# Performance work log

Hardware: AMD Instinct MI355X
Metric: run time of the kernel (lower is better)

## Reference

```python
import jax, jax.numpy as jnp
import numpy as np

B, S, HIDDEN, HEAD = 2, 2048, 1024, 16
CHUNK = HIDDEN // HEAD


def setup_inputs() -> dict:
    key = jax.random.key(0)
    ks = jax.random.split(key, 6)
    mk = lambda k, shape, std=1.0: jax.random.normal(k, shape, dtype=jnp.float32) * std
    return {
        "q": mk(ks[0], (B, S, HIDDEN)),
        "k": mk(ks[1], (B, S, HIDDEN)),
        "v": mk(ks[2], (B, S, HIDDEN)),
        "w_q": mk(ks[3], (HIDDEN, HIDDEN), 0.01),
        "w_k": mk(ks[4], (HIDDEN, HIDDEN), 0.01),
        "w_v": mk(ks[5], (HIDDEN, HIDDEN), 0.01),
    }


def _split_heads(x):
    # tf.stack(tf.split(x, head, axis=-1), axis=0): [B,S,HIDDEN] -> [HEAD,B,S,CHUNK]
    b, s, _ = x.shape
    return x.reshape(b, s, HEAD, CHUNK).transpose(2, 0, 1, 3)


def reference(q, k, v, w_q, w_k, w_v):
    emb_q = jnp.matmul(q, w_q)
    emb_k = jnp.matmul(k, w_k)
    emb_v = jnp.matmul(v, w_v)
    mq, mk, mv = _split_heads(emb_q), _split_heads(emb_k), _split_heads(emb_v)  # [H,B,S,C]
    scale = jnp.float32(CHUNK) ** 0.5
    scores = jnp.einsum("hbsc,hbtc->hbst", mq, mk) / scale  # [H,B,S,S]
    attn = jax.nn.softmax(scores, axis=-1)
    # post-softmax causal mask (band_part(-1, 0) == lower triangle) then renormalize
    s = attn.shape[-1]
    tril = jnp.tril(jnp.ones((s, s), dtype=attn.dtype))
    attn = attn * tril
    attn = attn / jnp.sum(attn, axis=3, keepdims=True)
    out = jnp.einsum("hbst,hbtc->hbsc", attn, mv)  # [H,B,S,C]
    # concat heads back on last axis: [H,B,S,C] -> [B,S,HIDDEN]
    return out.transpose(1, 2, 0, 3).reshape(q.shape[0], q.shape[1], HIDDEN)
```

## Files before the change

kernel.cpp:

```cpp
#include <hip/hip_runtime.h>
#include <stdint.h>

#define B_   2
#define S_   2048
#define HID  1024
#define NH   16
#define CH   64
#define MTOT (B_ * S_)
#define NELEM ((size_t)MTOT * HID)
#define WELEM ((size_t)HID * HID)

typedef unsigned short u16;
typedef unsigned int u32;
typedef __attribute__((ext_vector_type(4))) float f32x4;
typedef __attribute__((ext_vector_type(8))) short s16x8;
typedef __attribute__((ext_vector_type(4))) short s16x4;

__device__ __forceinline__ u16 f2bf(float f) {
  union { float f; unsigned u; } v; v.f = f;
  unsigned u = v.u;
  return (u16)((u + 0x7FFFu + ((u >> 16) & 1u)) >> 16);
}

__device__ __forceinline__ f32x4 mfma16(s16x8 a, s16x8 b, f32x4 c) {
  asm("v_mfma_f32_16x16x32_bf16 %0, %1, %2, %0" : "+v"(c) : "v"(a), "v"(b));
  return c;
}

__device__ __forceinline__ f32x4 mfma16z(s16x8 a, s16x8 b, f32x4 c) {
  f32x4 d;
  asm("v_mfma_f32_16x16x32_bf16 %0, %1, %2, %3"
      : "=&v"(d) : "v"(a), "v"(b), "v"(c));
  return d;
}

__device__ __forceinline__ f32x4 mfma16t(s16x8 a, s16x8 b, f32x4 c) {
  asm("v_mfma_f32_16x16x32_bf16 %0, %1, %2, %0" : "+&v"(c) : "v"(a), "v"(b));
  return c;
}

__device__ __forceinline__ f32x4 mfma16k16t(s16x4 a, s16x4 b, f32x4 c) {
  asm("v_mfma_f32_16x16x16_bf16 %0, %1, %2, %0" : "+&v"(c) : "v"(a), "v"(b));
  return c;
}

__device__ __forceinline__ u32 cvtpk(float lo, float hi) {
  u32 r;
  asm("v_cvt_pk_bf16_f32 %0, %1, %2" : "=v"(r) : "v"(lo), "v"(hi));
  return r;
}

__device__ __forceinline__ void mfma_fence() {
  asm volatile("s_nop 7\n\ts_nop 7\n\ts_nop 7" ::: );
}

__device__ __forceinline__ void gload_lds16(const u16* g, u16* l) {
  __builtin_amdgcn_global_load_lds((const __attribute__((address_space(1))) void*)g,
                                   (__attribute__((address_space(3))) void*)l,
                                   16, 0, 0);
}

__global__ __launch_bounds__(256) void k_transposeW(const float* __restrict__ w0,
                                                    const float* __restrict__ w1,
                                                    const float* __restrict__ w2,
                                                    u16* __restrict__ wT) {
  const float* w = (blockIdx.z == 0) ? w0 : (blockIdx.z == 1) ? w1 : w2;
  u16* o = wT + (size_t)blockIdx.z * WELEM;
  __shared__ u16 tile[64][65];
  int x = threadIdx.x & 63, y = threadIdx.x >> 6;
  int r0 = blockIdx.x * 64, c0 = blockIdx.y * 64;
#pragma unroll
  for (int i = 0; i < 16; ++i) {
    int r = i * 4 + y;
    tile[r][x] = f2bf(w[(size_t)(r0 + r) * HID + c0 + x]);
  }
  __syncthreads();
#pragma unroll
  for (int i = 0; i < 16; ++i) {
    int cc = i * 4 + y;
    o[(size_t)(c0 + cc) * HID + r0 + x] = tile[x][cc];
  }
}

__global__ __launch_bounds__(256) void k_gemm(const float* __restrict__ qf32,
                                              const float* __restrict__ kf32,
                                              const float* __restrict__ vf32,
                                              const u16* __restrict__ BTall,
                                              u16* __restrict__ Call,
                                              u16* __restrict__ Vfrag) {
  int lin = blockIdx.x;
  int xcd = lin & 7;
  int chunk = xcd * 96 + (lin >> 3);
  int zz = chunk >> 8;
  int rem = chunk & 255;
  int ty = rem >> 3;
  int tx = rem & 7;

  const float* Af = (zz == 0) ? qf32 : (zz == 1) ? kf32 : vf32;
  const u16* BT = BTall + (size_t)zz * WELEM;
  u16*       C  = Call  + (size_t)zz * NELEM;
  int row0 = ty * 128, col0 = tx * 128;

  __shared__ __align__(16) u16 sA[128 * 32];
  __shared__ __align__(16) u16 sB[128 * 32];

  int t = threadIdx.x;
  int wave = t >> 6, lane = t & 63;
  int lrow = lane & 15, lhi = lane >> 4;
  int wr = wave >> 1, wc = wave & 1;

  f32x4 acc[4][4] = {};

  for (int kt = 0; kt < HID; kt += 32) {
#pragma unroll
    for (int r = 0; r < 2; ++r) {
      int idx = r * 256 + t;
      int srow = idx >> 2, scol = (idx & 3) << 3;
      int ldsoff = (r * 256 + wave * 64) * 8;
      gload_lds16(BT + (size_t)(col0 + srow) * HID + kt + scol, sB + ldsoff);
      const float* ap = Af + (size_t)(row0 + srow) * HID + kt + scol;
      f32x4 a0 = *(const f32x4*)ap;
      f32x4 a1 = *(const f32x4*)(ap + 4);
      union { u32 u[4]; s16x8 v; } aw;
      aw.u[0] = cvtpk(a0[0], a0[1]);
      aw.u[1] = cvtpk(a0[2], a0[3]);
      aw.u[2] = cvtpk(a1[0], a1[1]);
      aw.u[3] = cvtpk(a1[2], a1[3]);
      *(s16x8*)&sA[idx * 8] = aw.v;
    }
    __syncthreads();
    s16x8 af[4], bfr[4];
#pragma unroll
    for (int m = 0; m < 4; ++m)
      af[m] = *(const s16x8*)&sA[(wr * 64 + m * 16 + lrow) * 32 + lhi * 8];
#pragma unroll
    for (int n = 0; n < 4; ++n)
      bfr[n] = *(const s16x8*)&sB[(wc * 64 + n * 16 + lrow) * 32 + lhi * 8];
#pragma unroll
    for (int m = 0; m < 4; ++m)
#pragma unroll
      for (int n = 0; n < 4; ++n)
        acc[m][n] = mfma16(af[m], bfr[n], acc[m][n]);
    __syncthreads();
  }
  mfma_fence();
  if (zz == 2) {
#pragma unroll
    for (int m = 0; m < 4; ++m)
#pragma unroll
      for (int n = 0; n < 4; ++n) {
        int rr = row0 + wr * 64 + m * 16 + lhi * 4;
        int cc = col0 + wc * 64 + n * 16 + lrow;
        int bb = rr >> 11, tt = rr & 2047;
        int hh = cc >> 6, chl = cc & 63;
        size_t off = ((size_t)(bb * NH + hh)) * ((size_t)CH * S_) +
                     (size_t)(((tt >> 4) * 4 + (chl >> 4)) * 256 +
                              ((tt >> 2) & 3) * 64 + (chl & 15) * 4);
        u32 w0 = (u32)f2bf(acc[m][n][0]) | ((u32)f2bf(acc[m][n][1]) << 16);
        u32 w1 = (u32)f2bf(acc[m][n][2]) | ((u32)f2bf(acc[m][n][3]) << 16);
        uint2 w; w.x = w0; w.y = w1;
        *(uint2*)&Vfrag[off] = w;
      }
  } else {
    float scl = (zz == 0) ? 0.125f * 1.44269504f : 1.0f;
#pragma unroll
    for (int m = 0; m < 4; ++m)
#pragma unroll
      for (int n = 0; n < 4; ++n)
#pragma unroll
        for (int j = 0; j < 4; ++j) {
          int rr = row0 + wr * 64 + m * 16 + lhi * 4 + j;
          int cc = col0 + wc * 64 + n * 16 + lrow;
          C[(size_t)rr * HID + cc] = f2bf(acc[m][n][j] * scl);
        }
  }
}

__global__ __launch_bounds__(512) void k_attn(const u16* __restrict__ eq,
                                              const u16* __restrict__ ek,
                                              const u16* __restrict__ vf,
                                              float* __restrict__ op0,
                                              float* __restrict__ op1,
                                              float* __restrict__ lp) {
  int bh = blockIdx.x;
  int b = bh >> 4, h = bh & 15;
  int yy = blockIdx.y;
  int qt = 15 - (yy >> 1);
  int half = yy & 1;
  int q0b = qt * 128;
  int wave = threadIdx.x >> 6, lane = threadIdx.x & 63;
  int lrow = lane & 15, lhi = lane >> 4;
  int q0w = q0b + wave * 16;

  __shared__ __align__(16) u16 sKV[16384];

  const u16* gK = ek + (size_t)(b * S_) * HID + h * CH;
  const u16* gV = vf + (size_t)bh * ((size_t)CH * S_);

  s16x8 qf[2];
  {
    size_t qbase = (size_t)(b * S_ + q0w + lrow) * HID + h * CH;
    qf[0] = *(const s16x8*)(eq + qbase + lhi * 8);
    qf[1] = *(const s16x8*)(eq + qbase + 32 + lhi * 8);
  }

  f32x4 o[4] = {};
  f32x4 zreg = {0.f, 0.f, 0.f, 0.f};
  float lsum = 0.0f;

  int lr8 = lane >> 3, slot = lane & 7;
  int co = ((slot ^ lr8) << 3);

  int kb_lane = lrow * 64 + ((lhi ^ (lrow & 7)) << 3);
  int vb_lane = lhi * 64 + lrow * 4;

  int nst = qt + 1;
  int sbase = half * nst;
  int tb0 = sbase * 64;

  gload_lds16(gK + (size_t)(tb0 + wave * 8 + lr8) * HID + co, &sKV[wave * 512]);
  gload_lds16(gV + (size_t)(tb0 >> 4) * 1024 + wave * 512 + lane * 8,
              &sKV[8192 + wave * 512]);

#define ATTN_STEP(ST, BUF)                                                     \
  {                                                                            \
    int tb = (sbase + (ST)) * 64;                                              \
    __syncthreads();                                                           \
    if ((ST) + 1 < nst) {                                                      \
      int tb2 = tb + 64;                                                       \
      gload_lds16(gK + (size_t)(tb2 + wave * 8 + lr8) * HID + co,              \
                  &sKV[(1 - (BUF)) * 4096 + wave * 512]);                      \
      gload_lds16(gV + (size_t)(tb2 >> 4) * 1024 + wave * 512 + lane * 8,      \
                  &sKV[8192 + (1 - (BUF)) * 4096 + wave * 512]);               \
    }                                                                          \
    if (tb <= q0w + 15) {                                                      \
      f32x4 p[4];                                                              \
      _Pragma("unroll")                                                        \
      for (int kvf = 0; kvf < 4; ++kvf) {                                      \
        s16x8 k0 = *(const s16x8*)&sKV[(BUF) * 4096 + kvf * 1024 + kb_lane];   \
        s16x8 k1 = *(const s16x8*)&sKV[(BUF) * 4096 + kvf * 1024 +             \
                                       (kb_lane ^ 32)];                        \
        p[kvf] = mfma16z(k0, qf[0], zreg);                                     \
        p[kvf] = mfma16t(k1, qf[1], p[kvf]);                                   \
      }                                                                        \
      mfma_fence();                                                            \
      bool need_mask = (tb + 63 > q0w);                                        \
      s16x4 pa[4];                                                             \
      _Pragma("unroll")                                                        \
      for (int kvf = 0; kvf < 4; ++kvf) {                                      \
        float e[4];                                                            \
        _Pragma("unroll")                                                      \
        for (int j = 0; j < 4; ++j) {                                          \
          float v = p[kvf][j];                                                 \
          if (need_mask && (tb + kvf * 16 + lhi * 4 + j > q0w + lrow))         \
            v = -3.0e38f;                                                      \
          e[j] = exp2f(v);                                                     \
        }                                                                      \
        lsum += (e[0] + e[1]) + (e[2] + e[3]);                                 \
        union { u32 u[2]; s16x4 v4; } pk;                                      \
        pk.u[0] = cvtpk(e[0], e[1]);                                           \
        pk.u[1] = cvtpk(e[2], e[3]);                                           \
        pa[kvf] = pk.v4;                                                       \
      }                                                                        \
      asm volatile("s_nop 1" :::);   \
      _Pragma("unroll")                                                        \
      for (int n = 0; n < 4; ++n)                                              \
        _Pragma("unroll")                                                      \
        for (int kvf = 0; kvf < 4; ++kvf) {                                    \
          s16x4 vfr = *(const s16x4*)&sKV[8192 + (BUF) * 4096 +                \
                                          (kvf * 4 + n) * 256 + vb_lane];      \
          o[n] = mfma16k16t(pa[kvf], vfr, o[n]);                               \
        }                                                                      \
    }                                                                          \
  }

  for (int st2 = 0; st2 < nst; st2 += 2) {
    ATTN_STEP(st2, 0);
    if (st2 + 1 < nst) ATTN_STEP(st2 + 1, 1);
  }
#undef ATTN_STEP

  mfma_fence();

  lsum += __shfl_xor(lsum, 16);
  lsum += __shfl_xor(lsum, 32);

  float* ob = half ? op1 : op0;
#pragma unroll
  for (int j = 0; j < 4; ++j) {
    int q = q0w + lhi * 4 + j;
    float* op = ob + (size_t)(b * S_ + q) * HID + h * CH + lrow;
#pragma unroll
    for (int n = 0; n < 4; ++n)
      op[n * 16] = o[n][j];
  }
  if (lhi == 0) {
    int q = q0w + lrow;
    lp[(((size_t)half * B_ + b) * S_ + q) * NH + h] = lsum;
  }
}

__global__ __launch_bounds__(256) void k_combine(float* __restrict__ out,
                                                 const float* __restrict__ p1,
                                                 const float* __restrict__ lp) {
  size_t i = ((size_t)blockIdx.x * 256 + threadIdx.x) * 4;
  size_t row = i >> 10;
  int h = (int)((i & 1023) >> 6);
  size_t b = row >> 11, s = row & 2047;
  float l0 = lp[((0 * B_ + b) * S_ + s) * NH + h];
  float l1 = lp[((1 * B_ + b) * S_ + s) * NH + h];
  float inv = 1.0f / (l0 + l1);
  f32x4 a = *(const f32x4*)(out + i);
  f32x4 c = *(const f32x4*)(p1 + i);
#pragma unroll
  for (int k = 0; k < 4; ++k) a[k] = (a[k] + c[k]) * inv;
  *(f32x4*)(out + i) = a;
}

extern "C" void kernel_launch(void* const* d_in, const int* in_sizes, int n_in,
                              void* d_out, int out_size, void* d_ws, size_t ws_size,
                              hipStream_t stream) {
  const float* q  = (const float*)d_in[0];
  const float* k  = (const float*)d_in[1];
  const float* v  = (const float*)d_in[2];
  const float* wq = (const float*)d_in[3];
  const float* wk = (const float*)d_in[4];
  const float* wv = (const float*)d_in[5];
  float* out = (float*)d_out;

  u16* qkv = (u16*)d_ws;
  u16* wT  = qkv + 3 * NELEM;
  u16* emb = wT + 3 * WELEM;
  u16* vfr = emb + 2 * NELEM;

  float* op1 = (float*)d_ws;
  float* lp  = op1 + NELEM;

  k_transposeW<<<dim3(16, 16, 3), 256, 0, stream>>>(wq, wk, wv, wT);
  k_gemm<<<dim3(768), 256, 0, stream>>>(q, k, v, wT, emb, vfr);
  k_attn<<<dim3(B_ * NH, 32), 512, 0, stream>>>(emb, emb + NELEM, vfr,
                                                out, op1, lp);
  k_combine<<<dim3(NELEM / (256 * 4)), 256, 0, stream>>>(out, op1, lp);
}
```

Baseline: 89.02 us.

## Double-buffer projection GEMM LDS tiles and XOR-swizzle the K slots

The QKV projection GEMM now keeps two LDS buffers for the A and B tiles. It issues the global loads for the next K-slice (async LDS load for B, register prefetch for A) before computing MFMAs on the current slice, and writes the converted A tile afterward. This cuts each iteration to one barrier instead of two. It also XOR-swizzles the 8-element K slots by row to reduce LDS bank conflicts on fragment reads. In exchange it doubles LDS use, adds prefetch registers, and relies on the barrier at loop top to cover the async B load for the next buffer.

```diff
diff --git a/kernel.cpp b/kernel.cpp
--- a/kernel.cpp
+++ b/kernel.cpp
@@ -101,8 +101,8 @@
   u16*       C  = Call  + (size_t)zz * NELEM;
   int row0 = ty * 128, col0 = tx * 128;
 
-  __shared__ __align__(16) u16 sA[128 * 32];
-  __shared__ __align__(16) u16 sB[128 * 32];
+  __shared__ __align__(16) u16 sA[2][128 * 32];
+  __shared__ __align__(16) u16 sB[2][128 * 32];
 
   int t = threadIdx.x;
   int wave = t >> 6, lane = t & 63;
@@ -111,38 +111,75 @@
 
   f32x4 acc[4][4] = {};
 
+  int kswz = (lhi ^ ((lrow >> 1) & 3)) << 3;
+
+#define STAGE_B(KT, BUF)                                                       \
+  _Pragma("unroll")                                                            \
+  for (int r = 0; r < 2; ++r) {                                                \
+    int idx = r * 256 + t;                                                     \
+    int srow = idx >> 2;                                                       \
+    int scol = (((idx & 3) ^ ((srow >> 1) & 3)) << 3);                         \
+    int ldsoff = (r * 256 + wave * 64) * 8;                                    \
+    gload_lds16(BT + (size_t)(col0 + srow) * HID + (KT) + scol,                \
+                &sB[BUF][0] + ldsoff);                                         \
+  }
+
+#define LOAD_A(KT)                                                             \
+  _Pragma("unroll")                                                            \
+  for (int r = 0; r < 2; ++r) {                                                \
+    int idx = r * 256 + t;                                                     \
+    const float* ap = Af + (size_t)(row0 + (idx >> 2)) * HID + (KT) +          \
+                      ((idx & 3) << 3);                                        \
+    areg0[r] = *(const f32x4*)ap;                                              \
+    areg1[r] = *(const f32x4*)(ap + 4);                                        \
+  }
+
+#define WRITE_A(BUF)                                                           \
+  _Pragma("unroll")                                                            \
+  for (int r = 0; r < 2; ++r) {                                                \
+    int idx = r * 256 + t;                                                     \
+    int srow = idx >> 2;                                                       \
+    int slot = (idx & 3) ^ ((srow >> 1) & 3);                                  \
+    union { u32 u[4]; s16x8 v; } aw;                                           \
+    aw.u[0] = cvtpk(areg0[r][0], areg0[r][1]);                                 \
+    aw.u[1] = cvtpk(areg0[r][2], areg0[r][3]);                                 \
+    aw.u[2] = cvtpk(areg1[r][0], areg1[r][1]);                                 \
+    aw.u[3] = cvtpk(areg1[r][2], areg1[r][3]);                                 \
+    *(s16x8*)&sA[BUF][srow * 32 + slot * 8] = aw.v;                            \
+  }
+
+  f32x4 areg0[2], areg1[2];
+  STAGE_B(0, 0);
+  LOAD_A(0);
+  WRITE_A(0);
+
   for (int kt = 0; kt < HID; kt += 32) {
-#pragma unroll
-    for (int r = 0; r < 2; ++r) {
-      int idx = r * 256 + t;
-      int srow = idx >> 2, scol = (idx & 3) << 3;
-      int ldsoff = (r * 256 + wave * 64) * 8;
-      gload_lds16(BT + (size_t)(col0 + srow) * HID + kt + scol, sB + ldsoff);
-      const float* ap = Af + (size_t)(row0 + srow) * HID + kt + scol;
-      f32x4 a0 = *(const f32x4*)ap;
-      f32x4 a1 = *(const f32x4*)(ap + 4);
-      union { u32 u[4]; s16x8 v; } aw;
-      aw.u[0] = cvtpk(a0[0], a0[1]);
-      aw.u[1] = cvtpk(a0[2], a0[3]);
-      aw.u[2] = cvtpk(a1[0], a1[1]);
-      aw.u[3] = cvtpk(a1[2], a1[3]);
-      *(s16x8*)&sA[idx * 8] = aw.v;
+    int cur = (kt >> 5) & 1;
+    __syncthreads();
+    bool more = (kt + 32) < HID;
+    if (more) {
+      STAGE_B(kt + 32, 1 - cur);
+      LOAD_A(kt + 32);
     }
-    __syncthreads();
     s16x8 af[4], bfr[4];
 #pragma unroll
     for (int m = 0; m < 4; ++m)
-      af[m] = *(const s16x8*)&sA[(wr * 64 + m * 16 + lrow) * 32 + lhi * 8];
+      af[m] = *(const s16x8*)&sA[cur][(wr * 64 + m * 16 + lrow) * 32 + kswz];
 #pragma unroll
     for (int n = 0; n < 4; ++n)
-      bfr[n] = *(const s16x8*)&sB[(wc * 64 + n * 16 + lrow) * 32 + lhi * 8];
+      bfr[n] = *(const s16x8*)&sB[cur][(wc * 64 + n * 16 + lrow) * 32 + kswz];
 #pragma unroll
     for (int m = 0; m < 4; ++m)
 #pragma unroll
       for (int n = 0; n < 4; ++n)
         acc[m][n] = mfma16(af[m], bfr[n], acc[m][n]);
-    __syncthreads();
-  }
+    if (more) {
+      WRITE_A(1 - cur);
+    }
+  }
+#undef STAGE_B
+#undef LOAD_A
+#undef WRITE_A
   mfma_fence();
   if (zz == 2) {
 #pragma unroll
```

After: 88.05 us. About the same (-1.1%).
